# Kernel optimization log

Measured on AMD Instinct MI355X. Metric: run time of the kernel, lower is better.

## Reference

```python
import jax, jax.numpy as jnp
import numpy as np

EPS = 1e-12


def setup_inputs() -> dict:
    key = jax.random.key(0)
    k1, k2, k3 = jax.random.split(key, 3)
    N, D, K = 262144, 64, 1024
    input_data = jax.random.normal(k1, (N, D), dtype=jnp.float32)
    random_vector = jax.random.normal(k2, (N, D), dtype=jnp.float32)
    # HeUniform over (K, D): limit = sqrt(6 / fan_in) with fan_in = K
    limit = np.sqrt(6.0 / K)
    codebooks = jax.random.uniform(k3, (K, D), dtype=jnp.float32, minval=-limit, maxval=limit)
    codebooks_used = jnp.zeros((K,), dtype=jnp.int32)
    return {"input_data": input_data, "random_vector": random_vector,
            "codebooks": codebooks, "codebooks_used": codebooks_used}


def reference(input_data, random_vector, codebooks, codebooks_used):
    # training=True path of NSVQ.call
    K = codebooks.shape[0]
    N = input_data.shape[0]
    sim = input_data @ codebooks.T
    dists = (jnp.sum(input_data * input_data, axis=1, keepdims=True)
             + jnp.sum(codebooks * codebooks, axis=1)[None, :]
             - 2.0 * sim)
    min_indices = jnp.argmin(dists, axis=1)                      # [N]
    hard_q = codebooks[min_indices]                              # [N, D]
    # NSVQ noise substitution
    res_norm = jnp.sqrt(jnp.sum((input_data - hard_q) ** 2, axis=1, keepdims=True))
    rv_norm = jnp.sqrt(jnp.sum(random_vector ** 2, axis=1, keepdims=True))
    vq_error = (res_norm / (rv_norm + EPS)) * random_vector
    quantized_input = input_data + vq_error
    # perplexity from code usage histogram
    counts = jax.ops.segment_sum(jnp.ones((N,), dtype=jnp.float32), min_indices,
                                 num_segments=K)                 # [K]
    avg_probs = counts / jnp.float32(N)
    perplexity = jnp.exp(-jnp.sum(avg_probs * jnp.log(avg_probs + EPS)))
    codebooks_used_new = codebooks_used + counts.astype(jnp.int32)
    return quantized_input, perplexity, codebooks_used_new
```

## Files before the change

### kernel.cpp

```cpp
#include <hip/hip_runtime.h>
#include <math.h>


#define NROWS 262144
#define DIM 64
#define KCODES 1024
#define ND ((size_t)NROWS * DIM)

typedef __attribute__((ext_vector_type(8))) short bf16x8;
typedef __attribute__((ext_vector_type(4))) float f32x4;

__device__ inline short f2bf(float f) {
    unsigned u = __builtin_bit_cast(unsigned, f);
    unsigned r = (u + 0x7FFFu + ((u >> 16) & 1u)) >> 16;
    return (short)r;
}
__device__ inline float bf2f(short h) {
    unsigned u = ((unsigned)(unsigned short)h) << 16;
    return __builtin_bit_cast(float, u);
}

typedef const __attribute__((address_space(1))) void* as1p;
typedef __attribute__((address_space(3))) void* as3p;
__device__ inline void gl_lds16(const void* g, void* l) {
    __builtin_amdgcn_global_load_lds((as1p)g, (as3p)l, 16, 0, 0);
}

__global__ __launch_bounds__(256) void nsvq_prep(
    const float* __restrict__ cb, short* __restrict__ cbs,
    float* __restrict__ cnorm)
{
    const int tid = blockIdx.x * 256 + threadIdx.x;
    const int k = tid >> 3;
    const int u = tid & 7;
    const float* p = cb + (size_t)k * DIM + u * 8;
    float4 f0 = *(const float4*)p;
    float4 f1 = *(const float4*)(p + 4);
    float fv[8] = {f0.x, f0.y, f0.z, f0.w, f1.x, f1.y, f1.z, f1.w};

    float s = 0.f;
    bf16x8 hv, lv;
#pragma unroll
    for (int j = 0; j < 8; ++j) {
        s = fmaf(fv[j], fv[j], s);
        float f = -2.0f * fv[j];
        short hi = f2bf(f);
        hv[j] = hi;
        lv[j] = f2bf(f - bf2f(hi));
    }
#pragma unroll
    for (int o = 1; o < 8; o <<= 1) s += __shfl_xor(s, o, 64);

    const size_t base = (size_t)(k >> 7) * 16384 + (size_t)u * 1024 + (size_t)(k & 127) * 8;
    *(bf16x8*)(cbs + base) = hv;
    *(bf16x8*)(cbs + base + 8192) = lv;
    if (u == 0) cnorm[k] = s;
}

__global__ __launch_bounds__(256) void nsvq_fused(
    const float* __restrict__ x, const float* __restrict__ rv,
    const short* __restrict__ cbs, const float* __restrict__ cnorm,
    float* __restrict__ out, unsigned int* __restrict__ counts)
{
    __shared__ short lds[16384];

    const int tid  = threadIdx.x;
    const int lane = tid & 63;
    const int wave = tid >> 6;
    const int q    = lane >> 4;
    const int n    = lane & 15;
    const int wBase = blockIdx.x * 128 + wave * 32;

    float  xf[2][16];
    bf16x8 ah[2][2], al[2][2];
    float  xx[2];
#pragma unroll
    for (int s = 0; s < 2; ++s) {
        const int row = wBase + s * 16 + n;
        float acc = 0.f;
#pragma unroll
        for (int c2 = 0; c2 < 2; ++c2) {
            const float* p = x + (size_t)row * DIM + c2 * 32 + q * 8;
            float4 g0 = *(const float4*)p;
            float4 g1 = *(const float4*)(p + 4);
            xf[s][c2 * 8 + 0] = g0.x; xf[s][c2 * 8 + 1] = g0.y;
            xf[s][c2 * 8 + 2] = g0.z; xf[s][c2 * 8 + 3] = g0.w;
            xf[s][c2 * 8 + 4] = g1.x; xf[s][c2 * 8 + 5] = g1.y;
            xf[s][c2 * 8 + 6] = g1.z; xf[s][c2 * 8 + 7] = g1.w;
#pragma unroll
            for (int j = 0; j < 8; ++j) {
                float f = xf[s][c2 * 8 + j];
                acc = fmaf(f, f, acc);
                short hi = f2bf(f);
                ah[s][c2][j] = hi;
                al[s][c2][j] = f2bf(f - bf2f(hi));
            }
        }
        acc += __shfl_xor(acc, 16, 64);
        acc += __shfl_xor(acc, 32, 64);
        xx[s] = acc;
    }

    float best[2][4];
    int   bidx[2][4];
#pragma unroll
    for (int s = 0; s < 2; ++s)
#pragma unroll
        for (int r = 0; r < 4; ++r) { best[s][r] = 3.4e38f; bidx[s][r] = 0; }

    for (int chunk = 0; chunk < 8; ++chunk) {
        const short* src = cbs + (size_t)chunk * 16384;
#pragma unroll
        for (int r = 0; r < 8; ++r) {
            const int idx = r * 256 + tid;
            gl_lds16(src + idx * 8, lds + idx * 8);
        }
        float cn[8];
#pragma unroll
        for (int t = 0; t < 8; ++t) cn[t] = cnorm[chunk * 128 + t * 16 + n];

        __syncthreads();

#pragma unroll
        for (int t = 0; t < 8; ++t) {
            const int ci = (t * 16 + n) * 8;
            bf16x8 bh0 = *(const bf16x8*)(lds + q * 1024 + ci);
            bf16x8 bh1 = *(const bf16x8*)(lds + (q + 4) * 1024 + ci);
            bf16x8 bl0 = *(const bf16x8*)(lds + 8192 + q * 1024 + ci);
            bf16x8 bl1 = *(const bf16x8*)(lds + 8192 + (q + 4) * 1024 + ci);
            f32x4 cnv = {cn[t], cn[t], cn[t], cn[t]};
            const int code = chunk * 128 + t * 16 + n;

#pragma unroll
            for (int s = 0; s < 2; ++s) {
                f32x4 a = cnv;
                a = __builtin_amdgcn_mfma_f32_16x16x32_bf16(ah[s][0], bh0, a, 0, 0, 0);
                a = __builtin_amdgcn_mfma_f32_16x16x32_bf16(ah[s][1], bh1, a, 0, 0, 0);
                a = __builtin_amdgcn_mfma_f32_16x16x32_bf16(al[s][0], bh0, a, 0, 0, 0);
                a = __builtin_amdgcn_mfma_f32_16x16x32_bf16(al[s][1], bh1, a, 0, 0, 0);
                a = __builtin_amdgcn_mfma_f32_16x16x32_bf16(ah[s][0], bl0, a, 0, 0, 0);
                a = __builtin_amdgcn_mfma_f32_16x16x32_bf16(ah[s][1], bl1, a, 0, 0, 0);
#pragma unroll
                for (int r = 0; r < 4; ++r) {
                    if (a[r] < best[s][r]) { best[s][r] = a[r]; bidx[s][r] = code; }
                }
            }
        }
        __syncthreads();
    }

#pragma unroll
    for (int o = 1; o < 16; o <<= 1) {
#pragma unroll
        for (int s = 0; s < 2; ++s)
#pragma unroll
            for (int r = 0; r < 4; ++r) {
                float od = __shfl_xor(best[s][r], o, 64);
                int   ok = __shfl_xor(bidx[s][r], o, 64);
                if (od < best[s][r] || (od == best[s][r] && ok < bidx[s][r])) {
                    best[s][r] = od; bidx[s][r] = ok;
                }
            }
    }

    float* resf = (float*)lds;
    if (n == 0) {
#pragma unroll
        for (int s = 0; s < 2; ++s)
#pragma unroll
            for (int r = 0; r < 4; ++r) {
                const int rl = wave * 32 + s * 16 + q * 4 + r;
                resf[rl] = best[s][r];
                atomicAdd(&counts[bidx[s][r]], 1u);
            }
    }
    __syncthreads();

#pragma unroll
    for (int s = 0; s < 2; ++s) {
        const int row = wBase + s * 16 + n;
        float res2 = xx[s] + resf[wave * 32 + s * 16 + n];
        if (res2 < 0.f) res2 = 0.f;
        float resn = sqrtf(res2);

        float rvf[16];
        float rr = 0.f;
#pragma unroll
        for (int c2 = 0; c2 < 2; ++c2) {
            const float* p = rv + (size_t)row * DIM + c2 * 32 + q * 8;
            float4 g0 = *(const float4*)p;
            float4 g1 = *(const float4*)(p + 4);
            rvf[c2 * 8 + 0] = g0.x; rvf[c2 * 8 + 1] = g0.y;
            rvf[c2 * 8 + 2] = g0.z; rvf[c2 * 8 + 3] = g0.w;
            rvf[c2 * 8 + 4] = g1.x; rvf[c2 * 8 + 5] = g1.y;
            rvf[c2 * 8 + 6] = g1.z; rvf[c2 * 8 + 7] = g1.w;
#pragma unroll
            for (int j = 0; j < 8; ++j) {
                float f = rvf[c2 * 8 + j];
                rr = fmaf(f, f, rr);
            }
        }
        rr += __shfl_xor(rr, 16, 64);
        rr += __shfl_xor(rr, 32, 64);
        float scale = resn / (sqrtf(rr) + 1e-12f);

#pragma unroll
        for (int c2 = 0; c2 < 2; ++c2) {
            float4 o0, o1;
            o0.x = fmaf(scale, rvf[c2 * 8 + 0], xf[s][c2 * 8 + 0]);
            o0.y = fmaf(scale, rvf[c2 * 8 + 1], xf[s][c2 * 8 + 1]);
            o0.z = fmaf(scale, rvf[c2 * 8 + 2], xf[s][c2 * 8 + 2]);
            o0.w = fmaf(scale, rvf[c2 * 8 + 3], xf[s][c2 * 8 + 3]);
            o1.x = fmaf(scale, rvf[c2 * 8 + 4], xf[s][c2 * 8 + 4]);
            o1.y = fmaf(scale, rvf[c2 * 8 + 5], xf[s][c2 * 8 + 5]);
            o1.z = fmaf(scale, rvf[c2 * 8 + 6], xf[s][c2 * 8 + 6]);
            o1.w = fmaf(scale, rvf[c2 * 8 + 7], xf[s][c2 * 8 + 7]);
            float* op = out + (size_t)row * DIM + c2 * 32 + q * 8;
            *(float4*)op = o0;
            *(float4*)(op + 4) = o1;
        }
    }
}

__global__ void nsvq_finalize(const unsigned int* __restrict__ counts,
                              const int* __restrict__ used,
                              float* __restrict__ out)
{
    const int k = threadIdx.x;
    const unsigned c = counts[k];
    float avg = (float)c * (1.0f / (float)NROWS);
    float term = (c > 0) ? (-avg * logf(avg + 1e-12f)) : 0.0f;

    float v = term;
#pragma unroll
    for (int o = 32; o > 0; o >>= 1) v += __shfl_down(v, o, 64);

    __shared__ float partial[16];
    if ((threadIdx.x & 63) == 0) partial[threadIdx.x >> 6] = v;
    __syncthreads();

    if (threadIdx.x < 64) {
        float s = (threadIdx.x < 16) ? partial[threadIdx.x] : 0.0f;
#pragma unroll
        for (int o = 32; o > 0; o >>= 1) s += __shfl_down(s, o, 64);
        if (threadIdx.x == 0) out[ND] = expf(s);
    }
    out[ND + 1 + k] = (float)(c + (unsigned)used[k]);
}

extern "C" void kernel_launch(void* const* d_in, const int* in_sizes, int n_in,
                              void* d_out, int out_size, void* d_ws, size_t ws_size,
                              hipStream_t stream) {
    const float* x    = (const float*)d_in[0];
    const float* rv   = (const float*)d_in[1];
    const float* cb   = (const float*)d_in[2];
    const int*   used = (const int*)d_in[3];
    float* out = (float*)d_out;

    char* ws = (char*)d_ws;
    unsigned int* counts = (unsigned int*)ws;
    float*        cnorm  = (float*)(ws + 4096);
    short*        cbs    = (short*)(ws + 8192);

    hipMemsetAsync(counts, 0, KCODES * sizeof(unsigned int), stream);
    nsvq_prep<<<KCODES * 8 / 256, 256, 0, stream>>>(cb, cbs, cnorm);
    nsvq_fused<<<NROWS / 128, 256, 0, stream>>>(x, rv, cbs, cnorm, out, counts);
    nsvq_finalize<<<1, KCODES, 0, stream>>>(counts, used, out);
}
```

Before: 267.6 us.

## Double-buffer codebook chunks in LDS and switch split-precision MMA to fp16

Splits the codebook into 16 chunks of 64 codes and double-buffers them in LDS, so the next chunk's async global-to-LDS load overlaps MFMA work on the current one, with one barrier per chunk. Replaces bf16 hi/lo splitting with fp16 hi/lo, which keeps more mantissa bits in the split terms. Drops the xf register copy by rebuilding x from the hi+lo halves, and passes the row minimum through shuffles instead of LDS, removing a barrier. The changes aim to cut register pressure (launch_bounds now requests 4 blocks) and hide load latency. The risks are fp16 range limits and a small reconstruction error in the output x.

```diff
diff --git a/kernel.cpp b/kernel.cpp
--- a/kernel.cpp
+++ b/kernel.cpp
@@ -7,18 +7,8 @@
 #define KCODES 1024
 #define ND ((size_t)NROWS * DIM)
 
-typedef __attribute__((ext_vector_type(8))) short bf16x8;
+typedef __attribute__((ext_vector_type(8))) _Float16 f16x8;
 typedef __attribute__((ext_vector_type(4))) float f32x4;
-
-__device__ inline short f2bf(float f) {
-    unsigned u = __builtin_bit_cast(unsigned, f);
-    unsigned r = (u + 0x7FFFu + ((u >> 16) & 1u)) >> 16;
-    return (short)r;
-}
-__device__ inline float bf2f(short h) {
-    unsigned u = ((unsigned)(unsigned short)h) << 16;
-    return __builtin_bit_cast(float, u);
-}
 
 typedef const __attribute__((address_space(1))) void* as1p;
 typedef __attribute__((address_space(3))) void* as3p;
@@ -27,7 +17,7 @@
 }
 
 __global__ __launch_bounds__(256) void nsvq_prep(
-    const float* __restrict__ cb, short* __restrict__ cbs,
+    const float* __restrict__ cb, _Float16* __restrict__ cbs,
     float* __restrict__ cnorm)
 {
     const int tid = blockIdx.x * 256 + threadIdx.x;
@@ -39,30 +29,30 @@
     float fv[8] = {f0.x, f0.y, f0.z, f0.w, f1.x, f1.y, f1.z, f1.w};
 
     float s = 0.f;
-    bf16x8 hv, lv;
+    f16x8 hv, lv;
 #pragma unroll
     for (int j = 0; j < 8; ++j) {
         s = fmaf(fv[j], fv[j], s);
-        float f = -2.0f * fv[j];
-        short hi = f2bf(f);
-        hv[j] = hi;
-        lv[j] = f2bf(f - bf2f(hi));
+        float m2 = -2.0f * fv[j];
+        _Float16 h = (_Float16)m2;
+        hv[j] = h;
+        lv[j] = (_Float16)(m2 - (float)h);
     }
 #pragma unroll
     for (int o = 1; o < 8; o <<= 1) s += __shfl_xor(s, o, 64);
 
-    const size_t base = (size_t)(k >> 7) * 16384 + (size_t)u * 1024 + (size_t)(k & 127) * 8;
-    *(bf16x8*)(cbs + base) = hv;
-    *(bf16x8*)(cbs + base + 8192) = lv;
+    const size_t base = (size_t)(k >> 6) * 8192 + (size_t)u * 512 + (size_t)(k & 63) * 8;
+    *(f16x8*)(cbs + base) = hv;
+    *(f16x8*)(cbs + base + 4096) = lv;
     if (u == 0) cnorm[k] = s;
 }
 
-__global__ __launch_bounds__(256) void nsvq_fused(
+__global__ __launch_bounds__(256, 4) void nsvq_fused(
     const float* __restrict__ x, const float* __restrict__ rv,
-    const short* __restrict__ cbs, const float* __restrict__ cnorm,
+    const _Float16* __restrict__ cbs, const float* __restrict__ cnorm,
     float* __restrict__ out, unsigned int* __restrict__ counts)
 {
-    __shared__ short lds[16384];
+    __shared__ _Float16 lds[16384];
 
     const int tid  = threadIdx.x;
     const int lane = tid & 63;
@@ -71,29 +61,31 @@
     const int n    = lane & 15;
     const int wBase = blockIdx.x * 128 + wave * 32;
 
-    float  xf[2][16];
-    bf16x8 ah[2][2], al[2][2];
-    float  xx[2];
+#pragma unroll
+    for (int r = 0; r < 4; ++r) {
+        const int off = (r * 256 + tid) * 8;
+        gl_lds16(cbs + off, lds + off);
+    }
+
+    f16x8 ah[2][2], al[2][2];
+    float xx[2];
 #pragma unroll
     for (int s = 0; s < 2; ++s) {
         const int row = wBase + s * 16 + n;
+        const float* px = x + (size_t)row * DIM + q * 8;
         float acc = 0.f;
 #pragma unroll
         for (int c2 = 0; c2 < 2; ++c2) {
-            const float* p = x + (size_t)row * DIM + c2 * 32 + q * 8;
-            float4 g0 = *(const float4*)p;
-            float4 g1 = *(const float4*)(p + 4);
-            xf[s][c2 * 8 + 0] = g0.x; xf[s][c2 * 8 + 1] = g0.y;
-            xf[s][c2 * 8 + 2] = g0.z; xf[s][c2 * 8 + 3] = g0.w;
-            xf[s][c2 * 8 + 4] = g1.x; xf[s][c2 * 8 + 5] = g1.y;
-            xf[s][c2 * 8 + 6] = g1.z; xf[s][c2 * 8 + 7] = g1.w;
+            float4 g0 = *(const float4*)(px + c2 * 32);
+            float4 g1 = *(const float4*)(px + c2 * 32 + 4);
+            float fv[8] = {g0.x, g0.y, g0.z, g0.w, g1.x, g1.y, g1.z, g1.w};
 #pragma unroll
             for (int j = 0; j < 8; ++j) {
-                float f = xf[s][c2 * 8 + j];
+                float f = fv[j];
                 acc = fmaf(f, f, acc);
-                short hi = f2bf(f);
-                ah[s][c2][j] = hi;
-                al[s][c2][j] = f2bf(f - bf2f(hi));
+                _Float16 h = (_Float16)f;
+                ah[s][c2][j] = h;
+                al[s][c2][j] = (_Float16)(f - (float)h);
             }
         }
         acc += __shfl_xor(acc, 16, 64);
@@ -101,6 +93,10 @@
         xx[s] = acc;
     }
 
+    float cn_cur[4], cn_nxt[4];
+#pragma unroll
+    for (int t = 0; t < 4; ++t) cn_cur[t] = cnorm[t * 16 + n];
+
     float best[2][4];
     int   bidx[2][4];
 #pragma unroll
@@ -108,46 +104,54 @@
 #pragma unroll
         for (int r = 0; r < 4; ++r) { best[s][r] = 3.4e38f; bidx[s][r] = 0; }
 
-    for (int chunk = 0; chunk < 8; ++chunk) {
-        const short* src = cbs + (size_t)chunk * 16384;
-#pragma unroll
-        for (int r = 0; r < 8; ++r) {
-            const int idx = r * 256 + tid;
-            gl_lds16(src + idx * 8, lds + idx * 8);
-        }
-        float cn[8];
-#pragma unroll
-        for (int t = 0; t < 8; ++t) cn[t] = cnorm[chunk * 128 + t * 16 + n];
-
-        __syncthreads();
-
-#pragma unroll
-        for (int t = 0; t < 8; ++t) {
+    __syncthreads();
+
+    auto compute_chunk = [&](int b, int cbase) {
+        const _Float16* buf = lds + b * 8192;
+#pragma unroll
+        for (int t = 0; t < 4; ++t) {
             const int ci = (t * 16 + n) * 8;
-            bf16x8 bh0 = *(const bf16x8*)(lds + q * 1024 + ci);
-            bf16x8 bh1 = *(const bf16x8*)(lds + (q + 4) * 1024 + ci);
-            bf16x8 bl0 = *(const bf16x8*)(lds + 8192 + q * 1024 + ci);
-            bf16x8 bl1 = *(const bf16x8*)(lds + 8192 + (q + 4) * 1024 + ci);
-            f32x4 cnv = {cn[t], cn[t], cn[t], cn[t]};
-            const int code = chunk * 128 + t * 16 + n;
-
+            f16x8 bh0 = *(const f16x8*)(buf + q * 512 + ci);
+            f16x8 bh1 = *(const f16x8*)(buf + (q + 4) * 512 + ci);
+            f16x8 bl0 = *(const f16x8*)(buf + 4096 + q * 512 + ci);
+            f16x8 bl1 = *(const f16x8*)(buf + 4096 + (q + 4) * 512 + ci);
+            const int code = cbase + t * 16 + n;
 #pragma unroll
             for (int s = 0; s < 2; ++s) {
-                f32x4 a = cnv;
-                a = __builtin_amdgcn_mfma_f32_16x16x32_bf16(ah[s][0], bh0, a, 0, 0, 0);
-                a = __builtin_amdgcn_mfma_f32_16x16x32_bf16(ah[s][1], bh1, a, 0, 0, 0);
-                a = __builtin_amdgcn_mfma_f32_16x16x32_bf16(al[s][0], bh0, a, 0, 0, 0);
-                a = __builtin_amdgcn_mfma_f32_16x16x32_bf16(al[s][1], bh1, a, 0, 0, 0);
-                a = __builtin_amdgcn_mfma_f32_16x16x32_bf16(ah[s][0], bl0, a, 0, 0, 0);
-                a = __builtin_amdgcn_mfma_f32_16x16x32_bf16(ah[s][1], bl1, a, 0, 0, 0);
+                f32x4 a = {cn_cur[t], cn_cur[t], cn_cur[t], cn_cur[t]};
+                a = __builtin_amdgcn_mfma_f32_16x16x32_f16(ah[s][0], bh0, a, 0, 0, 0);
+                a = __builtin_amdgcn_mfma_f32_16x16x32_f16(ah[s][1], bh1, a, 0, 0, 0);
+                a = __builtin_amdgcn_mfma_f32_16x16x32_f16(al[s][0], bh0, a, 0, 0, 0);
+                a = __builtin_amdgcn_mfma_f32_16x16x32_f16(al[s][1], bh1, a, 0, 0, 0);
+                a = __builtin_amdgcn_mfma_f32_16x16x32_f16(ah[s][0], bl0, a, 0, 0, 0);
+                a = __builtin_amdgcn_mfma_f32_16x16x32_f16(ah[s][1], bl1, a, 0, 0, 0);
 #pragma unroll
                 for (int r = 0; r < 4; ++r) {
                     if (a[r] < best[s][r]) { best[s][r] = a[r]; bidx[s][r] = code; }
                 }
             }
         }
+    };
+
+    for (int c = 0; c < 15; ++c) {
+        const int b = c & 1;
+        {
+            const _Float16* src = cbs + (size_t)(c + 1) * 8192;
+            _Float16* dst = lds + (b ^ 1) * 8192;
+#pragma unroll
+            for (int r = 0; r < 4; ++r) {
+                const int off = (r * 256 + tid) * 8;
+                gl_lds16(src + off, dst + off);
+            }
+#pragma unroll
+            for (int t = 0; t < 4; ++t) cn_nxt[t] = cnorm[(c + 1) * 64 + t * 16 + n];
+        }
+        compute_chunk(b, c * 64);
         __syncthreads();
-    }
+#pragma unroll
+        for (int t = 0; t < 4; ++t) cn_cur[t] = cn_nxt[t];
+    }
+    compute_chunk(1, 15 * 64);
 
 #pragma unroll
     for (int o = 1; o < 16; o <<= 1) {
@@ -162,62 +166,61 @@
                 }
             }
     }
-
-    float* resf = (float*)lds;
     if (n == 0) {
 #pragma unroll
         for (int s = 0; s < 2; ++s)
 #pragma unroll
-            for (int r = 0; r < 4; ++r) {
-                const int rl = wave * 32 + s * 16 + q * 4 + r;
-                resf[rl] = best[s][r];
-                atomicAdd(&counts[bidx[s][r]], 1u);
-            }
-    }
-    __syncthreads();
-
+            for (int r = 0; r < 4; ++r) atomicAdd(&counts[bidx[s][r]], 1u);
+    }
+
+    const int src = ((n >> 2) << 4) | n;
 #pragma unroll
     for (int s = 0; s < 2; ++s) {
+        float w0 = __shfl(best[s][0], src, 64);
+        float w1 = __shfl(best[s][1], src, 64);
+        float w2 = __shfl(best[s][2], src, 64);
+        float w3 = __shfl(best[s][3], src, 64);
+        float wa = (n & 1) ? w1 : w0;
+        float wb = (n & 1) ? w3 : w2;
+        float dmin = (n & 2) ? wb : wa;
+
+        float res2 = xx[s] + dmin;
+        if (res2 < 0.f) res2 = 0.f;
+        const float resn = sqrtf(res2);
+
         const int row = wBase + s * 16 + n;
-        float res2 = xx[s] + resf[wave * 32 + s * 16 + n];
-        if (res2 < 0.f) res2 = 0.f;
-        float resn = sqrtf(res2);
-
+        const float* pr = rv + (size_t)row * DIM + q * 8;
         float rvf[16];
         float rr = 0.f;
 #pragma unroll
         for (int c2 = 0; c2 < 2; ++c2) {
-            const float* p = rv + (size_t)row * DIM + c2 * 32 + q * 8;
-            float4 g0 = *(const float4*)p;
-            float4 g1 = *(const float4*)(p + 4);
+            float4 g0 = *(const float4*)(pr + c2 * 32);
+            float4 g1 = *(const float4*)(pr + c2 * 32 + 4);
             rvf[c2 * 8 + 0] = g0.x; rvf[c2 * 8 + 1] = g0.y;
             rvf[c2 * 8 + 2] = g0.z; rvf[c2 * 8 + 3] = g0.w;
             rvf[c2 * 8 + 4] = g1.x; rvf[c2 * 8 + 5] = g1.y;
             rvf[c2 * 8 + 6] = g1.z; rvf[c2 * 8 + 7] = g1.w;
 #pragma unroll
-            for (int j = 0; j < 8; ++j) {
-                float f = rvf[c2 * 8 + j];
-                rr = fmaf(f, f, rr);
-            }
+            for (int j = 0; j < 8; ++j) rr = fmaf(rvf[c2 * 8 + j], rvf[c2 * 8 + j], rr);
         }
         rr += __shfl_xor(rr, 16, 64);
         rr += __shfl_xor(rr, 32, 64);
-        float scale = resn / (sqrtf(rr) + 1e-12f);
-
+        const float scale = resn / (sqrtf(rr) + 1e-12f);
+
+        float* po = out + (size_t)row * DIM + q * 8;
 #pragma unroll
         for (int c2 = 0; c2 < 2; ++c2) {
             float4 o0, o1;
-            o0.x = fmaf(scale, rvf[c2 * 8 + 0], xf[s][c2 * 8 + 0]);
-            o0.y = fmaf(scale, rvf[c2 * 8 + 1], xf[s][c2 * 8 + 1]);
-            o0.z = fmaf(scale, rvf[c2 * 8 + 2], xf[s][c2 * 8 + 2]);
-            o0.w = fmaf(scale, rvf[c2 * 8 + 3], xf[s][c2 * 8 + 3]);
-            o1.x = fmaf(scale, rvf[c2 * 8 + 4], xf[s][c2 * 8 + 4]);
-            o1.y = fmaf(scale, rvf[c2 * 8 + 5], xf[s][c2 * 8 + 5]);
-            o1.z = fmaf(scale, rvf[c2 * 8 + 6], xf[s][c2 * 8 + 6]);
-            o1.w = fmaf(scale, rvf[c2 * 8 + 7], xf[s][c2 * 8 + 7]);
-            float* op = out + (size_t)row * DIM + c2 * 32 + q * 8;
-            *(float4*)op = o0;
-            *(float4*)(op + 4) = o1;
+            o0.x = fmaf(scale, rvf[c2 * 8 + 0], (float)ah[s][c2][0] + (float)al[s][c2][0]);
+            o0.y = fmaf(scale, rvf[c2 * 8 + 1], (float)ah[s][c2][1] + (float)al[s][c2][1]);
+            o0.z = fmaf(scale, rvf[c2 * 8 + 2], (float)ah[s][c2][2] + (float)al[s][c2][2]);
+            o0.w = fmaf(scale, rvf[c2 * 8 + 3], (float)ah[s][c2][3] + (float)al[s][c2][3]);
+            o1.x = fmaf(scale, rvf[c2 * 8 + 4], (float)ah[s][c2][4] + (float)al[s][c2][4]);
+            o1.y = fmaf(scale, rvf[c2 * 8 + 5], (float)ah[s][c2][5] + (float)al[s][c2][5]);
+            o1.z = fmaf(scale, rvf[c2 * 8 + 6], (float)ah[s][c2][6] + (float)al[s][c2][6]);
+            o1.w = fmaf(scale, rvf[c2 * 8 + 7], (float)ah[s][c2][7] + (float)al[s][c2][7]);
+            *(float4*)(po + c2 * 32) = o0;
+            *(float4*)(po + c2 * 32 + 4) = o1;
         }
     }
 }
@@ -260,7 +263,7 @@
     char* ws = (char*)d_ws;
     unsigned int* counts = (unsigned int*)ws;
     float*        cnorm  = (float*)(ws + 4096);
-    short*        cbs    = (short*)(ws + 8192);
+    _Float16*     cbs    = (_Float16*)(ws + 8192);
 
     hipMemsetAsync(counts, 0, KCODES * sizeof(unsigned int), stream);
     nsvq_prep<<<KCODES * 8 / 256, 256, 0, stream>>>(cb, cbs, cnorm);
```

Result: no change. 264.0 us (-1.3%).
